# Kernel optimization log

Measured on AMD Instinct MI355X. Metric: run time of the kernel, lower is better.

Reference implementation:

```python
import jax, jax.numpy as jnp
import numpy as np
from jax import lax


def setup_inputs() -> dict:
    key = jax.random.key(0)
    ks = jax.random.split(key, 5)
    D, S, T, B, H = 2, 48, 48, 32, 256
    std = 1.0 / np.sqrt(H)
    return {
        "src_input_seq": jax.random.normal(ks[0], (S, B, H), jnp.float32),
        "trg_input_seq": jax.random.normal(ks[1], (T, B, H), jnp.float32),
        "W": jax.random.uniform(ks[2], (D, H, H), jnp.float32, -std, std),
        "U": jax.random.uniform(ks[3], (D, 2 * H, H), jnp.float32, -std, std),
        "b": jax.random.uniform(ks[4], (D, 1, H), jnp.float32, -std, std),
    }


def _grid_layer(x, y, Wd, Ud, bd):
    # x, y: [S, T, B, H] per-cell inputs for this depth
    S, T, B, H = x.shape
    Ux, Uy = Ud[:H], Ud[H:]  # state = concat([state_x, state_y]) @ U

    def row_step(prev_row_hx, row_inputs):
        # prev_row_hx: [T, B, H] = h_x of row i-1 (state_x); zeros for i == 0
        x_row, y_row = row_inputs  # [T, B, H]

        def cell_step(left_hx, inp):
            # left_hx: [B, H] = h_x of cell (i, j-1) (state_y); zeros for j == 0
            up_hx, x_t, y_t = inp
            temp = up_hx @ Ux + left_hx @ Uy + bd  # [B, H]
            h_x = jnp.tanh(x_t @ Wd + temp)
            h_y = jnp.tanh(y_t @ Wd + temp)
            return h_x, (h_x, h_y)

        _, (hx_row, hy_row) = lax.scan(
            cell_step, jnp.zeros((B, H), x.dtype), (prev_row_hx, x_row, y_row)
        )
        return hx_row, (hx_row, hy_row)

    _, (HX, HY) = lax.scan(row_step, jnp.zeros((T, B, H), x.dtype), (x, y))
    return jnp.stack([HX, HY], axis=2)  # [S, T, 2, B, H]


def reference(src_input_seq, trg_input_seq, W, U, b):
    S, B, H = src_input_seq.shape
    T = trg_input_seq.shape[0]
    depth = W.shape[0]
    # depth-0 inputs: x_t = src[i] (same for all j), y_t = trg[j] (same for all i)
    xs = jnp.broadcast_to(src_input_seq[:, None], (S, T, B, H))
    ys = jnp.broadcast_to(trg_input_seq[None, :], (S, T, B, H))
    outs = []
    for d in range(depth):
        Hd = _grid_layer(xs, ys, W[d], U[d], b[d])  # [S, T, 2, B, H]
        outs.append(Hd)
        xs, ys = Hd[:, :, 0], Hd[:, :, 1]
    return jnp.stack(outs, axis=0)  # [depth, S, T, 2, B, H]
```

## Files before the change

### kernel.cpp

```cpp
#include <hip/hip_runtime.h>
#include <hip/hip_bf16.h>


typedef short short8 __attribute__((ext_vector_type(8)));
typedef float f32x4 __attribute__((ext_vector_type(4)));

static constexpr size_t UF_OFF    = 0;
static constexpr size_t WF_OFF    = 512u * 1024;
static constexpr size_t SRCW_OFF  = 768u * 1024;
static constexpr size_t TRGW_OFF  = SRCW_OFF + 48u * 32 * 256 * 4;
static constexpr size_t FLAG0_OFF = TRGW_OFF + 48u * 32 * 256 * 4;
static constexpr size_t FLAG1_OFF = FLAG0_OFF + 48u * 48 * 128;
static constexpr int    FSTRIDE   = 32;

#define MFMA16(a, b, c) __builtin_amdgcn_mfma_f32_16x16x32_bf16(a, b, c, 0, 0, 0)

__device__ __forceinline__ short f2bf(float f) {
  __hip_bfloat16 h = __float2bfloat16(f);
  return __builtin_bit_cast(short, h);
}

__device__ __forceinline__ size_t plane_off(int d, int s, int t, int c) {
  return (size_t)(((d * 48 + s) * 48 + t) * 2 + c) * 8192u;
}

__device__ __forceinline__ void wait_ge(int* p, int v) {
  while (__hip_atomic_load(p, __ATOMIC_RELAXED, __HIP_MEMORY_SCOPE_AGENT) < v)
    __builtin_amdgcn_s_sleep(1);
  asm volatile("" ::: "memory");
}

__device__ __forceinline__ void st_llc(float* p, float v) {
  __hip_atomic_store(p, v, __ATOMIC_RELAXED, __HIP_MEMORY_SCOPE_AGENT);
}

__device__ __forceinline__ float fast_tanh(float x) {
  float e = exp2f(x * 2.88539008f);
  return 1.f - __fdividef(2.f, e + 1.f);
}

__global__ void preswizzle(const float* __restrict__ U,
                           const float* __restrict__ W,
                           char* __restrict__ ws) {
  int gid = blockIdx.x * 256 + threadIdx.x;
  if (gid < 32768) {
    int r = gid >> 11;
    int d = r >> 3, nh = (r >> 2) & 1, w = r & 3;
    int c = gid & 2047;
    int f = c >> 6, lane = c & 63;
    int nt = f >> 4, ks = f & 15;
    int kbase = ks * 32 + (lane >> 4) * 8;
    int n = nh * 128 + w * 32 + nt * 16 + (lane & 15);
    const float* sp = U + (size_t)d * 512 * 256 + n;
    short8 v;
#pragma unroll
    for (int j = 0; j < 8; ++j) v[j] = f2bf(sp[(size_t)(kbase + j) * 256]);
    *(short8*)(ws + UF_OFF + (size_t)gid * 16) = v;
  } else {
    int idx = gid - 32768;
    int r = idx >> 10;
    int d = r >> 3, nh = (r >> 2) & 1, w = r & 3;
    int c = idx & 1023;
    int f = c >> 6, lane = c & 63;
    int nt = f >> 3, ks = f & 7;
    int kbase = ks * 32 + (lane >> 4) * 8;
    int n = nh * 128 + w * 32 + nt * 16 + (lane & 15);
    const float* sp = W + (size_t)d * 256 * 256 + n;
    short8 v;
#pragma unroll
    for (int j = 0; j < 8; ++j) v[j] = f2bf(sp[(size_t)(kbase + j) * 256]);
    *(short8*)(ws + WF_OFF + (size_t)idx * 16) = v;
  }
}

__global__ __launch_bounds__(256, 1) void precompute_xw(
    const float* __restrict__ src, const float* __restrict__ trg,
    const float* __restrict__ bvec, char* __restrict__ ws) {
  __shared__ __align__(16) char lds[32 * 528];
  const int bid = blockIdx.x;
  const int i = bid >> 1, nh = bid & 1;
  const int tid = threadIdx.x;
  const int w = tid >> 6, lane = tid & 63;
  const int alane = lane & 15, q = lane >> 4;

  short8 bw[2][8];
  {
    const char* wb = ws + WF_OFF + (size_t)(nh * 4 + w) * 16384u + (size_t)lane * 16;
#pragma unroll
    for (int nt = 0; nt < 2; ++nt)
#pragma unroll
      for (int ks = 0; ks < 8; ++ks)
        bw[nt][ks] = *(const short8*)(wb + (nt * 8 + ks) * 1024);
  }

  const float* plane = (i < 48) ? src + (size_t)i * 8192 : trg + (size_t)(i - 48) * 8192;
#pragma unroll
  for (int it = 0; it < 4; ++it) {
    int gid = it * 256 + tid;
    int row = gid >> 5, c = gid & 31;
    const float* p = plane + row * 256 + c * 8;
    short8 v;
#pragma unroll
    for (int j = 0; j < 8; ++j) v[j] = f2bf(p[j]);
    *(short8*)(lds + row * 528 + c * 16) = v;
  }
  __syncthreads();

  const f32x4 zf = {0.f, 0.f, 0.f, 0.f};
  f32x4 acc[2][2];
  acc[0][0] = zf; acc[0][1] = zf; acc[1][0] = zf; acc[1][1] = zf;
  const char* ar0 = lds + alane * 528 + q * 16;
  const char* ar1 = lds + (alane + 16) * 528 + q * 16;
#pragma unroll
  for (int ks = 0; ks < 8; ++ks) {
    short8 a0 = *(const short8*)(ar0 + ks * 64);
    short8 a1 = *(const short8*)(ar1 + ks * 64);
#pragma unroll
    for (int nt = 0; nt < 2; ++nt) {
      acc[0][nt] = MFMA16(a0, bw[nt][ks], acc[0][nt]);
      acc[1][nt] = MFMA16(a1, bw[nt][ks], acc[1][nt]);
    }
  }

  const int n0 = nh * 128 + w * 32 + alane;
  float bs[2] = {bvec[n0], bvec[n0 + 16]};
  float* dst = (float*)(ws + (i < 48 ? SRCW_OFF : TRGW_OFF)) +
               (size_t)(i < 48 ? i : i - 48) * 8192;
#pragma unroll
  for (int mt = 0; mt < 2; ++mt)
#pragma unroll
    for (int nt = 0; nt < 2; ++nt)
#pragma unroll
      for (int rr = 0; rr < 4; ++rr) {
        int row = mt * 16 + q * 4 + rr;
        dst[row * 256 + n0 + nt * 16] = acc[mt][nt][rr] + bs[nt];
      }
}

__global__ __launch_bounds__(512, 2) void grid_main(
    float* __restrict__ out, const float* __restrict__ bvec,
    char* __restrict__ ws) {
  __shared__ __align__(16) char lds[3 * 32 * 528];
  char* const buf0 = lds;
  char* const buf1 = lds + 32 * 528;
  char* const buf2 = lds + 2 * 32 * 528;

  const int bid = blockIdx.x;
  const int d = bid / 48;
  const int t = bid % 48;
  const int tid = threadIdx.x;
  const int wv = tid >> 6;
  const int nh = wv >> 2, w = wv & 3;
  const int lane = tid & 63;
  const int alane = lane & 15, q = lane >> 4;
  const int n0 = nh * 128 + w * 32 + alane;

  int* flag0 = (int*)(ws + FLAG0_OFF);
  int* flag1 = (int*)(ws + FLAG1_OFF);
  const float* SRCW = (const float*)(ws + SRCW_OFF);
  const float* TRGW = (const float*)(ws + TRGW_OFF);

  for (int i = tid; i < 32 * 528 / 4; i += 512) ((int*)buf0)[i] = 0;

  short8 bu[2][16];
  {
    const char* ub = ws + UF_OFF + (size_t)((d * 2 + nh) * 4 + w) * 32768u +
                     (size_t)lane * 16;
#pragma unroll
    for (int nt = 0; nt < 2; ++nt)
#pragma unroll
      for (int ks = 0; ks < 16; ++ks)
        bu[nt][ks] = *(const short8*)(ub + (nt * 16 + ks) * 1024);
  }

  const char* up0 = buf0 + alane * 528 + q * 16;
  const char* up1 = buf0 + (alane + 16) * 528 + q * 16;
  const char* l0  = buf1 + alane * 528 + q * 16;
  const char* l1  = buf1 + (alane + 16) * 528 + q * 16;
  const char* y0  = buf2 + alane * 528 + q * 16;
  const char* y1  = buf2 + (alane + 16) * 528 + q * 16;

  __syncthreads();

  if (d == 0) {
    float pfy[16];
    {
      const float* syp = TRGW + (size_t)t * 8192;
#pragma unroll
      for (int mt = 0; mt < 2; ++mt)
#pragma unroll
        for (int nt = 0; nt < 2; ++nt)
#pragma unroll
          for (int rr = 0; rr < 4; ++rr) {
            int row = mt * 16 + q * 4 + rr;
            pfy[(mt * 2 + nt) * 4 + rr] = syp[row * 256 + n0 + nt * 16];
          }
    }
    for (int s = 0; s < 48; ++s) {
      f32x4 accx[2][2], accy[2][2];
      {
        const float* sxp = SRCW + (size_t)s * 8192;
#pragma unroll
        for (int mt = 0; mt < 2; ++mt)
#pragma unroll
          for (int nt = 0; nt < 2; ++nt)
#pragma unroll
            for (int rr = 0; rr < 4; ++rr) {
              int row = mt * 16 + q * 4 + rr;
              accx[mt][nt][rr] = sxp[row * 256 + n0 + nt * 16];
              accy[mt][nt][rr] = pfy[(mt * 2 + nt) * 4 + rr];
            }
      }
      if (t > 0) {
        wait_ge(&flag0[(s * 48 + (t - 1)) * FSTRIDE], 8);
        const float* pl = out + plane_off(0, s, t - 1, 0);
#pragma unroll
        for (int it = 0; it < 2; ++it) {
          int gid = it * 512 + tid;
          int row = gid >> 5, c = gid & 31;
          const float* p = pl + row * 256 + c * 8;
          short8 v;
#pragma unroll
          for (int j = 0; j < 8; ++j) v[j] = f2bf(p[j]);
          *(short8*)(buf1 + row * 528 + c * 16) = v;
        }
      }
      __syncthreads();
#pragma unroll
      for (int ks = 0; ks < 8; ++ks) {
        short8 a0 = *(const short8*)(up0 + ks * 64);
        short8 a1 = *(const short8*)(up1 + ks * 64);
        accx[0][0] = MFMA16(a0, bu[0][ks], accx[0][0]);
        accx[0][1] = MFMA16(a0, bu[1][ks], accx[0][1]);
        accx[1][0] = MFMA16(a1, bu[0][ks], accx[1][0]);
        accx[1][1] = MFMA16(a1, bu[1][ks], accx[1][1]);
        accy[0][0] = MFMA16(a0, bu[0][ks], accy[0][0]);
        accy[0][1] = MFMA16(a0, bu[1][ks], accy[0][1]);
        accy[1][0] = MFMA16(a1, bu[0][ks], accy[1][0]);
        accy[1][1] = MFMA16(a1, bu[1][ks], accy[1][1]);
      }
      if (t > 0) {
#pragma unroll
        for (int ks = 0; ks < 8; ++ks) {
          short8 a0 = *(const short8*)(l0 + ks * 64);
          short8 a1 = *(const short8*)(l1 + ks * 64);
          accx[0][0] = MFMA16(a0, bu[0][8 + ks], accx[0][0]);
          accx[0][1] = MFMA16(a0, bu[1][8 + ks], accx[0][1]);
          accx[1][0] = MFMA16(a1, bu[0][8 + ks], accx[1][0]);
          accx[1][1] = MFMA16(a1, bu[1][8 + ks], accx[1][1]);
          accy[0][0] = MFMA16(a0, bu[0][8 + ks], accy[0][0]);
          accy[0][1] = MFMA16(a0, bu[1][8 + ks], accy[0][1]);
          accy[1][0] = MFMA16(a1, bu[0][8 + ks], accy[1][0]);
          accy[1][1] = MFMA16(a1, bu[1][8 + ks], accy[1][1]);
        }
      }
      float hx[16];
      {
        float* hxp = out + plane_off(0, s, t, 0);
        float* hyp = out + plane_off(0, s, t, 1);
#pragma unroll
        for (int mt = 0; mt < 2; ++mt)
#pragma unroll
          for (int nt = 0; nt < 2; ++nt)
#pragma unroll
            for (int rr = 0; rr < 4; ++rr) {
              int row = mt * 16 + q * 4 + rr;
              int n = n0 + nt * 16;
              float xv = fast_tanh(accx[mt][nt][rr]);
              float yv = fast_tanh(accy[mt][nt][rr]);
              hx[(mt * 2 + nt) * 4 + rr] = xv;
              st_llc(&hxp[row * 256 + n], xv);
              st_llc(&hyp[row * 256 + n], yv);
            }
      }
      asm volatile("s_waitcnt vmcnt(0)" ::: "memory");
      if (lane == 0)
        __hip_atomic_fetch_add(&flag0[(s * 48 + t) * FSTRIDE], 1,
                               __ATOMIC_RELAXED, __HIP_MEMORY_SCOPE_AGENT);
      __syncthreads();
#pragma unroll
      for (int mt = 0; mt < 2; ++mt)
#pragma unroll
        for (int nt = 0; nt < 2; ++nt)
#pragma unroll
          for (int rr = 0; rr < 4; ++rr) {
            int row = mt * 16 + q * 4 + rr;
            *(short*)(buf0 + row * 528 + (n0 + nt * 16) * 2) =
                f2bf(hx[(mt * 2 + nt) * 4 + rr]);
          }
      __syncthreads();
    }
  } else {
    const char* wb = ws + WF_OFF + (size_t)((2 + nh) * 4 + w) * 16384u +
                     (size_t)lane * 16;
    const float bsa = bvec[256 + n0], bsb = bvec[256 + n0 + 16];
    const f32x4 bA = {bsa, bsa, bsa, bsa};
    const f32x4 bB = {bsb, bsb, bsb, bsb};
    const f32x4 zf = {0.f, 0.f, 0.f, 0.f};
    for (int s = 0; s < 48; ++s) {
      f32x4 accx[2][2], accy[2][2], acc[2][2];
      accx[0][0] = bA; accx[0][1] = bB; accx[1][0] = bA; accx[1][1] = bB;
      accy[0][0] = bA; accy[0][1] = bB; accy[1][0] = bA; accy[1][1] = bB;
      acc[0][0] = zf; acc[0][1] = zf; acc[1][0] = zf; acc[1][1] = zf;

      wait_ge(&flag0[(s * 48 + t) * FSTRIDE], 8);
      {
        const float* px = out + plane_off(0, s, t, 0);
        const float* py = out + plane_off(0, s, t, 1);
#pragma unroll
        for (int it = 0; it < 4; ++it) {
          int gid = it * 512 + tid;
          int pidx = gid >> 10, row = (gid >> 5) & 31, c = gid & 31;
          const float* pp = pidx ? py : px;
          char* db = pidx ? buf2 : buf1;
          const float* p = pp + row * 256 + c * 8;
          short8 v;
#pragma unroll
          for (int j = 0; j < 8; ++j) v[j] = f2bf(p[j]);
          *(short8*)(db + row * 528 + c * 16) = v;
        }
      }
      __syncthreads();
#pragma unroll
      for (int ks = 0; ks < 8; ++ks) {
        short8 b0 = *(const short8*)(wb + ks * 1024);
        short8 b1 = *(const short8*)(wb + (8 + ks) * 1024);
        short8 ax0 = *(const short8*)(l0 + ks * 64);
        short8 ax1 = *(const short8*)(l1 + ks * 64);
        short8 ay0 = *(const short8*)(y0 + ks * 64);
        short8 ay1 = *(const short8*)(y1 + ks * 64);
        accx[0][0] = MFMA16(ax0, b0, accx[0][0]);
        accx[0][1] = MFMA16(ax0, b1, accx[0][1]);
        accx[1][0] = MFMA16(ax1, b0, accx[1][0]);
        accx[1][1] = MFMA16(ax1, b1, accx[1][1]);
        accy[0][0] = MFMA16(ay0, b0, accy[0][0]);
        accy[0][1] = MFMA16(ay0, b1, accy[0][1]);
        accy[1][0] = MFMA16(ay1, b0, accy[1][0]);
        accy[1][1] = MFMA16(ay1, b1, accy[1][1]);
      }
      if (t > 0) wait_ge(&flag1[(s * 48 + (t - 1)) * FSTRIDE], 8);
      __syncthreads();
      if (t > 0) {
        const float* pl = out + plane_off(1, s, t - 1, 0);
#pragma unroll
        for (int it = 0; it < 2; ++it) {
          int gid = it * 512 + tid;
          int row = gid >> 5, c = gid & 31;
          const float* p = pl + row * 256 + c * 8;
          short8 v;
#pragma unroll
          for (int j = 0; j < 8; ++j) v[j] = f2bf(p[j]);
          *(short8*)(buf1 + row * 528 + c * 16) = v;
        }
      }
      __syncthreads();
#pragma unroll
      for (int ks = 0; ks < 8; ++ks) {
        short8 a0 = *(const short8*)(up0 + ks * 64);
        short8 a1 = *(const short8*)(up1 + ks * 64);
        acc[0][0] = MFMA16(a0, bu[0][ks], acc[0][0]);
        acc[0][1] = MFMA16(a0, bu[1][ks], acc[0][1]);
        acc[1][0] = MFMA16(a1, bu[0][ks], acc[1][0]);
        acc[1][1] = MFMA16(a1, bu[1][ks], acc[1][1]);
      }
      if (t > 0) {
#pragma unroll
        for (int ks = 0; ks < 8; ++ks) {
          short8 a0 = *(const short8*)(l0 + ks * 64);
          short8 a1 = *(const short8*)(l1 + ks * 64);
          acc[0][0] = MFMA16(a0, bu[0][8 + ks], acc[0][0]);
          acc[0][1] = MFMA16(a0, bu[1][8 + ks], acc[0][1]);
          acc[1][0] = MFMA16(a1, bu[0][8 + ks], acc[1][0]);
          acc[1][1] = MFMA16(a1, bu[1][8 + ks], acc[1][1]);
        }
      }
      float hx[16];
      {
        float* hxp = out + plane_off(1, s, t, 0);
        float* hyp = out + plane_off(1, s, t, 1);
#pragma unroll
        for (int mt = 0; mt < 2; ++mt)
#pragma unroll
          for (int nt = 0; nt < 2; ++nt)
#pragma unroll
            for (int rr = 0; rr < 4; ++rr) {
              int row = mt * 16 + q * 4 + rr;
              int n = n0 + nt * 16;
              float tv = acc[mt][nt][rr];
              float xv = fast_tanh(accx[mt][nt][rr] + tv);
              float yv = fast_tanh(accy[mt][nt][rr] + tv);
              hx[(mt * 2 + nt) * 4 + rr] = xv;
              st_llc(&hxp[row * 256 + n], xv);
              hyp[row * 256 + n] = yv;
            }
      }
      asm volatile("s_waitcnt vmcnt(0)" ::: "memory");
      if (lane == 0)
        __hip_atomic_fetch_add(&flag1[(s * 48 + t) * FSTRIDE], 1,
                               __ATOMIC_RELAXED, __HIP_MEMORY_SCOPE_AGENT);
      __syncthreads();
#pragma unroll
      for (int mt = 0; mt < 2; ++mt)
#pragma unroll
        for (int nt = 0; nt < 2; ++nt)
#pragma unroll
          for (int rr = 0; rr < 4; ++rr) {
            int row = mt * 16 + q * 4 + rr;
            *(short*)(buf0 + row * 528 + (n0 + nt * 16) * 2) =
                f2bf(hx[(mt * 2 + nt) * 4 + rr]);
          }
      __syncthreads();
    }
  }
}

extern "C" void kernel_launch(void* const* d_in, const int* in_sizes, int n_in,
                              void* d_out, int out_size, void* d_ws, size_t ws_size,
                              hipStream_t stream) {
  const float* src = (const float*)d_in[0];
  const float* trg = (const float*)d_in[1];
  const float* W   = (const float*)d_in[2];
  const float* U   = (const float*)d_in[3];
  const float* bv  = (const float*)d_in[4];
  float* out = (float*)d_out;
  char* ws = (char*)d_ws;

  hipMemsetAsync(ws + FLAG0_OFF, 0, 2u * 48 * 48 * 128, stream);
  preswizzle<<<192, 256, 0, stream>>>(U, W, ws);
  precompute_xw<<<192, 256, 0, stream>>>(src, trg, bv, ws);
  grid_main<<<96, 512, 0, stream>>>(out, bv, ws);
}
```

Before: 901.8 us.

## Shorten recurrence critical path with split flags and shared U-matmul accumulator

Computes the shared state term (up/left h_x times U) once into a common accumulator instead of duplicating the MFMAs for both the x and y outputs. Issues the global loads of the left neighbour's h_x before the up-direction MFMAs so their latency overlaps compute. Uses a separate LDS buffer for the depth-1 left input so one barrier can be dropped. Publishes h_x under its own flag before h_y is written, so dependent blocks can start sooner. Also stores precomputed input projections in a fragment-native layout so each thread reads them as vector loads. Launch bounds drop to one block per CU and LDS grows, which lowers possible occupancy and may cost latency hiding.

```diff
diff --git a/kernel.cpp b/kernel.cpp
--- a/kernel.cpp
+++ b/kernel.cpp
@@ -11,7 +11,6 @@
 static constexpr size_t TRGW_OFF  = SRCW_OFF + 48u * 32 * 256 * 4;
 static constexpr size_t FLAG0_OFF = TRGW_OFF + 48u * 32 * 256 * 4;
 static constexpr size_t FLAG1_OFF = FLAG0_OFF + 48u * 48 * 128;
-static constexpr int    FSTRIDE   = 32;
 
 #define MFMA16(a, b, c) __builtin_amdgcn_mfma_f32_16x16x32_bf16(a, b, c, 0, 0, 0)
 
@@ -22,6 +21,10 @@
 
 __device__ __forceinline__ size_t plane_off(int d, int s, int t, int c) {
   return (size_t)(((d * 48 + s) * 48 + t) * 2 + c) * 8192u;
+}
+
+__device__ __forceinline__ int* flagp(char* ws, size_t off, int s, int t) {
+  return (int*)(ws + off) + (size_t)(s * 48 + t) * 32;
 }
 
 __device__ __forceinline__ void wait_ge(int* p, int v) {
@@ -124,26 +127,27 @@
 
   const int n0 = nh * 128 + w * 32 + alane;
   float bs[2] = {bvec[n0], bvec[n0 + 16]};
+  const int gtid = (nh * 4 + w) * 64 + lane;
   float* dst = (float*)(ws + (i < 48 ? SRCW_OFF : TRGW_OFF)) +
-               (size_t)(i < 48 ? i : i - 48) * 8192;
+               (size_t)(i < 48 ? i : i - 48) * 8192 + (size_t)gtid * 16;
 #pragma unroll
   for (int mt = 0; mt < 2; ++mt)
 #pragma unroll
-    for (int nt = 0; nt < 2; ++nt)
-#pragma unroll
-      for (int rr = 0; rr < 4; ++rr) {
-        int row = mt * 16 + q * 4 + rr;
-        dst[row * 256 + n0 + nt * 16] = acc[mt][nt][rr] + bs[nt];
-      }
-}
-
-__global__ __launch_bounds__(512, 2) void grid_main(
+    for (int nt = 0; nt < 2; ++nt) {
+      f32x4 v = acc[mt][nt];
+      v[0] += bs[nt]; v[1] += bs[nt]; v[2] += bs[nt]; v[3] += bs[nt];
+      ((f32x4*)dst)[mt * 2 + nt] = v;
+    }
+}
+
+__global__ __launch_bounds__(512, 1) void grid_main(
     float* __restrict__ out, const float* __restrict__ bvec,
     char* __restrict__ ws) {
-  __shared__ __align__(16) char lds[3 * 32 * 528];
+  __shared__ __align__(16) char lds[4 * 32 * 528];
   char* const buf0 = lds;
   char* const buf1 = lds + 32 * 528;
   char* const buf2 = lds + 2 * 32 * 528;
+  char* const buf3 = lds + 3 * 32 * 528;
 
   const int bid = blockIdx.x;
   const int d = bid / 48;
@@ -155,12 +159,8 @@
   const int alane = lane & 15, q = lane >> 4;
   const int n0 = nh * 128 + w * 32 + alane;
 
-  int* flag0 = (int*)(ws + FLAG0_OFF);
-  int* flag1 = (int*)(ws + FLAG1_OFF);
   const float* SRCW = (const float*)(ws + SRCW_OFF);
   const float* TRGW = (const float*)(ws + TRGW_OFF);
-
-  for (int i = tid; i < 32 * 528 / 4; i += 512) ((int*)buf0)[i] = 0;
 
   short8 bu[2][16];
   {
@@ -172,6 +172,9 @@
       for (int ks = 0; ks < 16; ++ks)
         bu[nt][ks] = *(const short8*)(ub + (nt * 16 + ks) * 1024);
   }
+
+  for (int z = tid; z < 32 * 528 / 4; z += 512) ((int*)buf0)[z] = 0;
+  __syncthreads();
 
   const char* up0 = buf0 + alane * 528 + q * 16;
   const char* up1 = buf0 + (alane + 16) * 528 + q * 16;
@@ -179,131 +182,135 @@
   const char* l1  = buf1 + (alane + 16) * 528 + q * 16;
   const char* y0  = buf2 + alane * 528 + q * 16;
   const char* y1  = buf2 + (alane + 16) * 528 + q * 16;
-
-  __syncthreads();
+  const char* m0  = buf3 + alane * 528 + q * 16;
+  const char* m1  = buf3 + (alane + 16) * 528 + q * 16;
+  const f32x4 zf = {0.f, 0.f, 0.f, 0.f};
 
   if (d == 0) {
-    float pfy[16];
+    f32x4 pfy[4];
     {
-      const float* syp = TRGW + (size_t)t * 8192;
-#pragma unroll
-      for (int mt = 0; mt < 2; ++mt)
-#pragma unroll
-        for (int nt = 0; nt < 2; ++nt)
-#pragma unroll
-          for (int rr = 0; rr < 4; ++rr) {
-            int row = mt * 16 + q * 4 + rr;
-            pfy[(mt * 2 + nt) * 4 + rr] = syp[row * 256 + n0 + nt * 16];
-          }
+      const f32x4* py = (const f32x4*)(TRGW + (size_t)t * 8192 + (size_t)tid * 16);
+      pfy[0] = py[0]; pfy[1] = py[1]; pfy[2] = py[2]; pfy[3] = py[3];
     }
     for (int s = 0; s < 48; ++s) {
-      f32x4 accx[2][2], accy[2][2];
-      {
-        const float* sxp = SRCW + (size_t)s * 8192;
-#pragma unroll
-        for (int mt = 0; mt < 2; ++mt)
-#pragma unroll
-          for (int nt = 0; nt < 2; ++nt)
-#pragma unroll
-            for (int rr = 0; rr < 4; ++rr) {
-              int row = mt * 16 + q * 4 + rr;
-              accx[mt][nt][rr] = sxp[row * 256 + n0 + nt * 16];
-              accy[mt][nt][rr] = pfy[(mt * 2 + nt) * 4 + rr];
-            }
-      }
+      f32x4 accx[2][2], accy[2][2], accT[2][2];
+      {
+        const f32x4* px = (const f32x4*)(SRCW + (size_t)s * 8192 + (size_t)tid * 16);
+        accx[0][0] = px[0]; accx[0][1] = px[1]; accx[1][0] = px[2]; accx[1][1] = px[3];
+      }
+      accy[0][0] = pfy[0]; accy[0][1] = pfy[1]; accy[1][0] = pfy[2]; accy[1][1] = pfy[3];
+      accT[0][0] = zf; accT[0][1] = zf; accT[1][0] = zf; accT[1][1] = zf;
+
+      f32x4 lva[2], lvb[2];
       if (t > 0) {
-        wait_ge(&flag0[(s * 48 + (t - 1)) * FSTRIDE], 8);
+        wait_ge(flagp(ws, FLAG0_OFF, s, t - 1), 8);
         const float* pl = out + plane_off(0, s, t - 1, 0);
 #pragma unroll
         for (int it = 0; it < 2; ++it) {
           int gid = it * 512 + tid;
           int row = gid >> 5, c = gid & 31;
           const float* p = pl + row * 256 + c * 8;
-          short8 v;
-#pragma unroll
-          for (int j = 0; j < 8; ++j) v[j] = f2bf(p[j]);
-          *(short8*)(buf1 + row * 528 + c * 16) = v;
-        }
-      }
-      __syncthreads();
+          lva[it] = *(const f32x4*)p;
+          lvb[it] = *(const f32x4*)(p + 4);
+        }
+      }
 #pragma unroll
       for (int ks = 0; ks < 8; ++ks) {
         short8 a0 = *(const short8*)(up0 + ks * 64);
         short8 a1 = *(const short8*)(up1 + ks * 64);
-        accx[0][0] = MFMA16(a0, bu[0][ks], accx[0][0]);
-        accx[0][1] = MFMA16(a0, bu[1][ks], accx[0][1]);
-        accx[1][0] = MFMA16(a1, bu[0][ks], accx[1][0]);
-        accx[1][1] = MFMA16(a1, bu[1][ks], accx[1][1]);
-        accy[0][0] = MFMA16(a0, bu[0][ks], accy[0][0]);
-        accy[0][1] = MFMA16(a0, bu[1][ks], accy[0][1]);
-        accy[1][0] = MFMA16(a1, bu[0][ks], accy[1][0]);
-        accy[1][1] = MFMA16(a1, bu[1][ks], accy[1][1]);
-      }
+        accT[0][0] = MFMA16(a0, bu[0][ks], accT[0][0]);
+        accT[0][1] = MFMA16(a0, bu[1][ks], accT[0][1]);
+        accT[1][0] = MFMA16(a1, bu[0][ks], accT[1][0]);
+        accT[1][1] = MFMA16(a1, bu[1][ks], accT[1][1]);
+      }
+      if (t > 0) {
+#pragma unroll
+        for (int it = 0; it < 2; ++it) {
+          int gid = it * 512 + tid;
+          int row = gid >> 5, c = gid & 31;
+          short8 v;
+#pragma unroll
+          for (int j = 0; j < 4; ++j) {
+            v[j] = f2bf(lva[it][j]);
+            v[4 + j] = f2bf(lvb[it][j]);
+          }
+          *(short8*)(buf1 + row * 528 + c * 16) = v;
+        }
+      }
+      __syncthreads();
       if (t > 0) {
 #pragma unroll
         for (int ks = 0; ks < 8; ++ks) {
           short8 a0 = *(const short8*)(l0 + ks * 64);
           short8 a1 = *(const short8*)(l1 + ks * 64);
-          accx[0][0] = MFMA16(a0, bu[0][8 + ks], accx[0][0]);
-          accx[0][1] = MFMA16(a0, bu[1][8 + ks], accx[0][1]);
-          accx[1][0] = MFMA16(a1, bu[0][8 + ks], accx[1][0]);
-          accx[1][1] = MFMA16(a1, bu[1][8 + ks], accx[1][1]);
-          accy[0][0] = MFMA16(a0, bu[0][8 + ks], accy[0][0]);
-          accy[0][1] = MFMA16(a0, bu[1][8 + ks], accy[0][1]);
-          accy[1][0] = MFMA16(a1, bu[0][8 + ks], accy[1][0]);
-          accy[1][1] = MFMA16(a1, bu[1][8 + ks], accy[1][1]);
-        }
-      }
-      float hx[16];
+          accT[0][0] = MFMA16(a0, bu[0][8 + ks], accT[0][0]);
+          accT[0][1] = MFMA16(a0, bu[1][8 + ks], accT[0][1]);
+          accT[1][0] = MFMA16(a1, bu[0][8 + ks], accT[1][0]);
+          accT[1][1] = MFMA16(a1, bu[1][8 + ks], accT[1][1]);
+        }
+      }
+      float hxv[16];
       {
         float* hxp = out + plane_off(0, s, t, 0);
-        float* hyp = out + plane_off(0, s, t, 1);
 #pragma unroll
         for (int mt = 0; mt < 2; ++mt)
 #pragma unroll
           for (int nt = 0; nt < 2; ++nt)
 #pragma unroll
             for (int rr = 0; rr < 4; ++rr) {
-              int row = mt * 16 + q * 4 + rr;
-              int n = n0 + nt * 16;
-              float xv = fast_tanh(accx[mt][nt][rr]);
-              float yv = fast_tanh(accy[mt][nt][rr]);
-              hx[(mt * 2 + nt) * 4 + rr] = xv;
-              st_llc(&hxp[row * 256 + n], xv);
-              st_llc(&hyp[row * 256 + n], yv);
+              int i = (mt * 2 + nt) * 4 + rr;
+              int row = mt * 16 + q * 4 + rr, c = n0 + nt * 16;
+              float xv = fast_tanh(accx[mt][nt][rr] + accT[mt][nt][rr]);
+              hxv[i] = xv;
+              st_llc(&hxp[row * 256 + c], xv);
             }
       }
       asm volatile("s_waitcnt vmcnt(0)" ::: "memory");
       if (lane == 0)
-        __hip_atomic_fetch_add(&flag0[(s * 48 + t) * FSTRIDE], 1,
+        __hip_atomic_fetch_add(flagp(ws, FLAG0_OFF, s, t), 1,
                                __ATOMIC_RELAXED, __HIP_MEMORY_SCOPE_AGENT);
-      __syncthreads();
+      {
+        float* hyp = out + plane_off(0, s, t, 1);
+#pragma unroll
+        for (int mt = 0; mt < 2; ++mt)
+#pragma unroll
+          for (int nt = 0; nt < 2; ++nt)
+#pragma unroll
+            for (int rr = 0; rr < 4; ++rr) {
+              int row = mt * 16 + q * 4 + rr, c = n0 + nt * 16;
+              st_llc(&hyp[row * 256 + c],
+                     fast_tanh(accy[mt][nt][rr] + accT[mt][nt][rr]));
+            }
+      }
+      asm volatile("s_waitcnt vmcnt(0)" ::: "memory");
+      if (lane == 0)
+        __hip_atomic_fetch_add(flagp(ws, FLAG0_OFF, s, t) + 1, 1,
+                               __ATOMIC_RELAXED, __HIP_MEMORY_SCOPE_AGENT);
 #pragma unroll
       for (int mt = 0; mt < 2; ++mt)
 #pragma unroll
         for (int nt = 0; nt < 2; ++nt)
 #pragma unroll
           for (int rr = 0; rr < 4; ++rr) {
-            int row = mt * 16 + q * 4 + rr;
-            *(short*)(buf0 + row * 528 + (n0 + nt * 16) * 2) =
-                f2bf(hx[(mt * 2 + nt) * 4 + rr]);
+            int row = mt * 16 + q * 4 + rr, c = n0 + nt * 16;
+            *(short*)(buf0 + row * 528 + c * 2) = f2bf(hxv[(mt * 2 + nt) * 4 + rr]);
           }
       __syncthreads();
     }
   } else {
-    const char* wb = ws + WF_OFF + (size_t)((2 + nh) * 4 + w) * 16384u +
-                     (size_t)lane * 16;
+    const char* wbp = ws + WF_OFF + (size_t)((2 + nh) * 4 + w) * 16384u +
+                      (size_t)lane * 16;
     const float bsa = bvec[256 + n0], bsb = bvec[256 + n0 + 16];
     const f32x4 bA = {bsa, bsa, bsa, bsa};
     const f32x4 bB = {bsb, bsb, bsb, bsb};
-    const f32x4 zf = {0.f, 0.f, 0.f, 0.f};
     for (int s = 0; s < 48; ++s) {
-      f32x4 accx[2][2], accy[2][2], acc[2][2];
+      f32x4 accx[2][2], accy[2][2], accT[2][2];
       accx[0][0] = bA; accx[0][1] = bB; accx[1][0] = bA; accx[1][1] = bB;
       accy[0][0] = bA; accy[0][1] = bB; accy[1][0] = bA; accy[1][1] = bB;
-      acc[0][0] = zf; acc[0][1] = zf; acc[1][0] = zf; acc[1][1] = zf;
-
-      wait_ge(&flag0[(s * 48 + t) * FSTRIDE], 8);
+      accT[0][0] = zf; accT[0][1] = zf; accT[1][0] = zf; accT[1][1] = zf;
+
+      wait_ge(flagp(ws, FLAG0_OFF, s, t) + 1, 8);
+      f32x4 xva[4], xvb[4];
       {
         const float* px = out + plane_off(0, s, t, 0);
         const float* py = out + plane_off(0, s, t, 1);
@@ -311,20 +318,40 @@
         for (int it = 0; it < 4; ++it) {
           int gid = it * 512 + tid;
           int pidx = gid >> 10, row = (gid >> 5) & 31, c = gid & 31;
-          const float* pp = pidx ? py : px;
+          const float* pp = (pidx ? py : px) + row * 256 + c * 8;
+          xva[it] = *(const f32x4*)pp;
+          xvb[it] = *(const f32x4*)(pp + 4);
+        }
+      }
+#pragma unroll
+      for (int ks = 0; ks < 8; ++ks) {
+        short8 a0 = *(const short8*)(up0 + ks * 64);
+        short8 a1 = *(const short8*)(up1 + ks * 64);
+        accT[0][0] = MFMA16(a0, bu[0][ks], accT[0][0]);
+        accT[0][1] = MFMA16(a0, bu[1][ks], accT[0][1]);
+        accT[1][0] = MFMA16(a1, bu[0][ks], accT[1][0]);
+        accT[1][1] = MFMA16(a1, bu[1][ks], accT[1][1]);
+      }
+      {
+#pragma unroll
+        for (int it = 0; it < 4; ++it) {
+          int gid = it * 512 + tid;
+          int pidx = gid >> 10, row = (gid >> 5) & 31, c = gid & 31;
           char* db = pidx ? buf2 : buf1;
-          const float* p = pp + row * 256 + c * 8;
           short8 v;
 #pragma unroll
-          for (int j = 0; j < 8; ++j) v[j] = f2bf(p[j]);
+          for (int j = 0; j < 4; ++j) {
+            v[j] = f2bf(xva[it][j]);
+            v[4 + j] = f2bf(xvb[it][j]);
+          }
           *(short8*)(db + row * 528 + c * 16) = v;
         }
       }
       __syncthreads();
 #pragma unroll
       for (int ks = 0; ks < 8; ++ks) {
-        short8 b0 = *(const short8*)(wb + ks * 1024);
-        short8 b1 = *(const short8*)(wb + (8 + ks) * 1024);
+        short8 b0 = *(const short8*)(wbp + ks * 1024);
+        short8 b1 = *(const short8*)(wbp + (8 + ks) * 1024);
         short8 ax0 = *(const short8*)(l0 + ks * 64);
         short8 ax1 = *(const short8*)(l1 + ks * 64);
         short8 ay0 = *(const short8*)(y0 + ks * 64);
@@ -338,76 +365,84 @@
         accy[1][0] = MFMA16(ay1, b0, accy[1][0]);
         accy[1][1] = MFMA16(ay1, b1, accy[1][1]);
       }
-      if (t > 0) wait_ge(&flag1[(s * 48 + (t - 1)) * FSTRIDE], 8);
+      if (t > 0) {
+        wait_ge(flagp(ws, FLAG1_OFF, s, t - 1), 8);
+        const float* pl = out + plane_off(1, s, t - 1, 0);
+        f32x4 lva[2], lvb[2];
+#pragma unroll
+        for (int it = 0; it < 2; ++it) {
+          int gid = it * 512 + tid;
+          int row = gid >> 5, c = gid & 31;
+          const float* p = pl + row * 256 + c * 8;
+          lva[it] = *(const f32x4*)p;
+          lvb[it] = *(const f32x4*)(p + 4);
+        }
+#pragma unroll
+        for (int it = 0; it < 2; ++it) {
+          int gid = it * 512 + tid;
+          int row = gid >> 5, c = gid & 31;
+          short8 v;
+#pragma unroll
+          for (int j = 0; j < 4; ++j) {
+            v[j] = f2bf(lva[it][j]);
+            v[4 + j] = f2bf(lvb[it][j]);
+          }
+          *(short8*)(buf3 + row * 528 + c * 16) = v;
+        }
+      }
       __syncthreads();
       if (t > 0) {
-        const float* pl = out + plane_off(1, s, t - 1, 0);
-#pragma unroll
-        for (int it = 0; it < 2; ++it) {
-          int gid = it * 512 + tid;
-          int row = gid >> 5, c = gid & 31;
-          const float* p = pl + row * 256 + c * 8;
-          short8 v;
-#pragma unroll
-          for (int j = 0; j < 8; ++j) v[j] = f2bf(p[j]);
-          *(short8*)(buf1 + row * 528 + c * 16) = v;
-        }
-      }
-      __syncthreads();
-#pragma unroll
-      for (int ks = 0; ks < 8; ++ks) {
-        short8 a0 = *(const short8*)(up0 + ks * 64);
-        short8 a1 = *(const short8*)(up1 + ks * 64);
-        acc[0][0] = MFMA16(a0, bu[0][ks], acc[0][0]);
-        acc[0][1] = MFMA16(a0, bu[1][ks], acc[0][1]);
-        acc[1][0] = MFMA16(a1, bu[0][ks], acc[1][0]);
-        acc[1][1] = MFMA16(a1, bu[1][ks], acc[1][1]);
-      }
-      if (t > 0) {
 #pragma unroll
         for (int ks = 0; ks < 8; ++ks) {
-          short8 a0 = *(const short8*)(l0 + ks * 64);
-          short8 a1 = *(const short8*)(l1 + ks * 64);
-          acc[0][0] = MFMA16(a0, bu[0][8 + ks], acc[0][0]);
-          acc[0][1] = MFMA16(a0, bu[1][8 + ks], acc[0][1]);
-          acc[1][0] = MFMA16(a1, bu[0][8 + ks], acc[1][0]);
-          acc[1][1] = MFMA16(a1, bu[1][8 + ks], acc[1][1]);
-        }
-      }
-      float hx[16];
+          short8 a0 = *(const short8*)(m0 + ks * 64);
+          short8 a1 = *(const short8*)(m1 + ks * 64);
+          accT[0][0] = MFMA16(a0, bu[0][8 + ks], accT[0][0]);
+          accT[0][1] = MFMA16(a0, bu[1][8 + ks], accT[0][1]);
+          accT[1][0] = MFMA16(a1, bu[0][8 + ks], accT[1][0]);
+          accT[1][1] = MFMA16(a1, bu[1][8 + ks], accT[1][1]);
+        }
+      }
+      float hxv[16];
       {
         float* hxp = out + plane_off(1, s, t, 0);
-        float* hyp = out + plane_off(1, s, t, 1);
 #pragma unroll
         for (int mt = 0; mt < 2; ++mt)
 #pragma unroll
           for (int nt = 0; nt < 2; ++nt)
 #pragma unroll
             for (int rr = 0; rr < 4; ++rr) {
-              int row = mt * 16 + q * 4 + rr;
-              int n = n0 + nt * 16;
-              float tv = acc[mt][nt][rr];
-              float xv = fast_tanh(accx[mt][nt][rr] + tv);
-              float yv = fast_tanh(accy[mt][nt][rr] + tv);
-              hx[(mt * 2 + nt) * 4 + rr] = xv;
-              st_llc(&hxp[row * 256 + n], xv);
-              hyp[row * 256 + n] = yv;
+              int i = (mt * 2 + nt) * 4 + rr;
+              int row = mt * 16 + q * 4 + rr, c = n0 + nt * 16;
+              float xv = fast_tanh(accx[mt][nt][rr] + accT[mt][nt][rr]);
+              hxv[i] = xv;
+              st_llc(&hxp[row * 256 + c], xv);
             }
       }
       asm volatile("s_waitcnt vmcnt(0)" ::: "memory");
       if (lane == 0)
-        __hip_atomic_fetch_add(&flag1[(s * 48 + t) * FSTRIDE], 1,
+        __hip_atomic_fetch_add(flagp(ws, FLAG1_OFF, s, t), 1,
                                __ATOMIC_RELAXED, __HIP_MEMORY_SCOPE_AGENT);
-      __syncthreads();
+      {
+        float* hyp = out + plane_off(1, s, t, 1);
+#pragma unroll
+        for (int mt = 0; mt < 2; ++mt)
+#pragma unroll
+          for (int nt = 0; nt < 2; ++nt)
+#pragma unroll
+            for (int rr = 0; rr < 4; ++rr) {
+              int row = mt * 16 + q * 4 + rr, c = n0 + nt * 16;
+              hyp[row * 256 + c] =
+                  fast_tanh(accy[mt][nt][rr] + accT[mt][nt][rr]);
+            }
+      }
 #pragma unroll
       for (int mt = 0; mt < 2; ++mt)
 #pragma unroll
         for (int nt = 0; nt < 2; ++nt)
 #pragma unroll
           for (int rr = 0; rr < 4; ++rr) {
-            int row = mt * 16 + q * 4 + rr;
-            *(short*)(buf0 + row * 528 + (n0 + nt * 16) * 2) =
-                f2bf(hx[(mt * 2 + nt) * 4 + rr]);
+            int row = mt * 16 + q * 4 + rr, c = n0 + nt * 16;
+            *(short*)(buf0 + row * 528 + c * 2) = f2bf(hxv[(mt * 2 + nt) * 4 + rr]);
           }
       __syncthreads();
     }
```

After: 816.8 us. 1.1x faster.
